# Optimization experiments

Measured on AMD Instinct MI355X. Metric: run time of the kernel, lower is better.

The kernel has to match this reference:

```python
import jax, jax.numpy as jnp
import numpy as np

B, S, D = 2, 2048, 1024
H = 16
HD = D // H  # head_dim = 64


def _xavier(key, shape):
    fan_out, fan_in = shape
    bound = jnp.sqrt(6.0 / (fan_in + fan_out))
    return jax.random.uniform(key, shape, jnp.float32, -bound, bound)


def setup_inputs() -> dict:
    key = jax.random.key(0)
    kx, kqkv, ko = jax.random.split(key, 3)
    x = jax.random.normal(kx, (B, S, D), jnp.float32)
    # torch nn.Linear stores weight as [out, in]; we keep that layout and use x @ W.T
    W_qkv = _xavier(kqkv, (3 * D, D))
    b_qkv = jnp.zeros((3 * D,), jnp.float32)
    W_o = _xavier(ko, (D, D))
    b_o = jnp.zeros((D,), jnp.float32)
    return {"x": x, "W_qkv": W_qkv, "b_qkv": b_qkv, "W_o": W_o, "b_o": b_o}


def reference(x, W_qkv, b_qkv, W_o, b_o):
    b, s, d = x.shape
    h, hd = H, HD
    # qkv projection: [b, s, 3d]
    qkv = jnp.einsum("bsd,ed->bse", x, W_qkv) + b_qkv
    # [b, s, h, 3*hd] -> [b, h, s, 3*hd]
    qkv = qkv.reshape(b, s, h, 3 * hd).transpose(0, 2, 1, 3)
    q, k, v = jnp.split(qkv, 3, axis=-1)
    scale = 1.0 / jnp.sqrt(jnp.asarray(hd, x.dtype))
    logits = jnp.einsum("bhqd,bhkd->bhqk", q, k) * scale
    attn = jax.nn.softmax(logits, axis=-1)
    values = jnp.einsum("bhqk,bhkd->bhqd", attn, v)
    values = values.transpose(0, 2, 1, 3).reshape(b, s, d)
    return jnp.einsum("bsd,ed->bse", values, W_o) + b_o
```

## Files before the change

kernel.cpp:

```cpp
#include <hip/hip_runtime.h>

typedef unsigned short u16;
typedef __attribute__((ext_vector_type(8))) short bf16x8;
typedef __attribute__((ext_vector_type(4))) float f32x4;
typedef __attribute__((ext_vector_type(16))) float f32x16;
typedef __attribute__((ext_vector_type(4))) unsigned short u16x4;

__device__ __forceinline__ u16 f2bf(float f) {
    unsigned u = __float_as_uint(f);
    u = u + 0x7FFFu + ((u >> 16) & 1u);
    return (u16)(u >> 16);
}

__device__ __forceinline__ void gload16(const void* g, void* l) {
    __builtin_amdgcn_global_load_lds(
        (const __attribute__((address_space(1))) unsigned int*)g,
        (__attribute__((address_space(3))) unsigned int*)l,
        16, 0, 0);
}

__device__ __forceinline__ f32x4 mfma16(bf16x8 a, bf16x8 b, f32x4 c) {
    return __builtin_amdgcn_mfma_f32_16x16x32_bf16(a, b, c, 0, 0, 0);
}
__device__ __forceinline__ f32x16 mfma32(bf16x8 a, bf16x8 b, f32x16 c) {
    return __builtin_amdgcn_mfma_f32_32x32x16_bf16(a, b, c, 0, 0, 0);
}

__global__ __launch_bounds__(256) void cvt_all(const float* __restrict__ x,
                                               const float* __restrict__ wqkv,
                                               const float* __restrict__ wo,
                                               u16* __restrict__ dst) {
    int i = blockIdx.x * 256 + threadIdx.x;
    float4 v;
    if (i < 1048576)       v = ((const float4*)x)[i];
    else if (i < 1835008)  v = ((const float4*)wqkv)[i - 1048576];
    else                   v = ((const float4*)wo)[i - 1835008];
    u16x4 o = { f2bf(v.x), f2bf(v.y), f2bf(v.z), f2bf(v.w) };
    ((u16x4*)dst)[i] = o;
}

template <int BM, int BN, bool OUT_BF16>
__global__ __launch_bounds__(256) void gemm_bt(const u16* __restrict__ A,
                                               const u16* __restrict__ Bm,
                                               const float* __restrict__ bias,
                                               void* __restrict__ Cp,
                                               int M, int N, int K) {
    constexpr int FM = BM / 32, FN = BN / 32;
    __shared__ u16 As[2][BM * 64];
    __shared__ u16 Bs[2][BN * 64];
    const int tid = threadIdx.x, lane = tid & 63, wave = tid >> 6;
    const int wr = wave >> 1, wc = wave & 1;
    const int l15 = lane & 15, l4 = lane >> 4;

    const int nx = gridDim.x, nwg = nx * gridDim.y;
    const int id = blockIdx.y * nx + blockIdx.x;
    const int wg = (id & 7) * (nwg >> 3) + (id >> 3);
    const int m0 = (wg / nx) * BM, n0 = (wg % nx) * BN;

    f32x4 zero = {0.f, 0.f, 0.f, 0.f};
    f32x4 acc[FM][FN];
#pragma unroll
    for (int m = 0; m < FM; ++m)
#pragma unroll
        for (int n = 0; n < FN; ++n) acc[m][n] = zero;

#define STAGE_BT(tt, buf) {                                                 \
    _Pragma("unroll")                                                       \
    for (int i = 0; i < BM / 32; ++i) {                                     \
        int c = i * 256 + tid;                                              \
        int r = c >> 3, kc = (c & 7) ^ (r & 7);                             \
        gload16(A + (size_t)(m0 + r) * K + (tt) * 64 + kc * 8,              \
                &As[buf][(i * 256 + wave * 64) * 8]);                       \
    }                                                                       \
    _Pragma("unroll")                                                       \
    for (int i = 0; i < BN / 32; ++i) {                                     \
        int c = i * 256 + tid;                                              \
        int r = c >> 3, kc = (c & 7) ^ (r & 7);                             \
        gload16(Bm + (size_t)(n0 + r) * K + (tt) * 64 + kc * 8,             \
                &Bs[buf][(i * 256 + wave * 64) * 8]);                       \
    } }

    const int nt = K >> 6;
    STAGE_BT(0, 0);
    for (int t = 0; t < nt; ++t) {
        asm volatile("s_waitcnt vmcnt(0)" ::: "memory");
        asm volatile("s_barrier" ::: "memory");
        if (t < nt - 1) { STAGE_BT(t + 1, (t + 1) & 1); }
        const char* Asb = (const char*)As[t & 1];
        const char* Bsb = (const char*)Bs[t & 1];
#pragma unroll
        for (int kk = 0; kk < 2; ++kk) {
            bf16x8 af[FM], bfr[FN];
#pragma unroll
            for (int m = 0; m < FM; ++m) {
                int row = wr * (BM / 2) + m * 16 + l15;
                int ch = (kk * 4 + l4) ^ (row & 7);
                af[m] = *(const bf16x8*)(Asb + row * 128 + ch * 16);
            }
#pragma unroll
            for (int n = 0; n < FN; ++n) {
                int row = wc * (BN / 2) + n * 16 + l15;
                int ch = (kk * 4 + l4) ^ (row & 7);
                bfr[n] = *(const bf16x8*)(Bsb + row * 128 + ch * 16);
            }
#pragma unroll
            for (int m = 0; m < FM; ++m)
#pragma unroll
                for (int n = 0; n < FN; ++n)
                    acc[m][n] = mfma16(af[m], bfr[n], acc[m][n]);
        }
    }
#undef STAGE_BT
    float bv[FN];
#pragma unroll
    for (int n = 0; n < FN; ++n) bv[n] = bias[n0 + wc * (BN / 2) + n * 16 + l15];
#pragma unroll
    for (int m = 0; m < FM; ++m) {
#pragma unroll
        for (int j = 0; j < 4; ++j) {
            size_t row = (size_t)(m0 + wr * (BM / 2) + m * 16 + l4 * 4 + j);
#pragma unroll
            for (int n = 0; n < FN; ++n) {
                int col = n0 + wc * (BN / 2) + n * 16 + l15;
                float v = acc[m][n][j] + bv[n];
                if (OUT_BF16)
                    ((u16*)Cp)[row * (size_t)N + col] = f2bf(v);
                else
                    ((float*)Cp)[row * (size_t)N + col] = v;
            }
        }
    }
}

__global__ __launch_bounds__(512) void gemm192(const u16* __restrict__ A,
                                               const u16* __restrict__ Bm,
                                               const float* __restrict__ bias,
                                               u16* __restrict__ Cp,
                                               u16* __restrict__ Vt,
                                               int M, int N, int K) {
    __shared__ __align__(16) char lds[114688];
    const int tid = threadIdx.x, lane = tid & 63, wave = tid >> 6;
    const int wr = wave >> 2, wc = wave & 3;
    const int l15 = lane & 15, l4 = lane >> 4;

    const int nx = gridDim.x, nwg = nx * gridDim.y;
    const int id = blockIdx.y * nx + blockIdx.x;
    const int wg = (id & 7) * (nwg >> 3) + (id >> 3);
    const int m0 = (wg / nx) * 256, n0 = (wg % nx) * 192;

    const u16* asrc[2][2];
#pragma unroll
    for (int q = 0; q < 2; ++q)
#pragma unroll
        for (int r = 0; r < 2; ++r) {
            int c = r * 512 + tid;
            int lr = c >> 3;
            int kc = (c & 7) ^ (lr & 7);
            asrc[q][r] = A + (size_t)(m0 + lr + (lr & 64) + q * 64) * K + kc * 8;
        }
    const u16* bsrc[3];
    {
        int lr2 = tid >> 3;
        int kc = (tid & 7) ^ (lr2 & 7);
#pragma unroll
        for (int r3 = 0; r3 < 3; ++r3)
            bsrc[r3] = Bm + (size_t)(n0 + r3 * 64 + lr2) * K + kc * 8;
    }
    const int sd0 = wave * 1024;
    const int sd1 = 8192 + wave * 1024;

    const int roA = (wr * 64 + l15) * 128;
    const int roB = (wc * 16 + l15) * 128;
    int ch16[2];
#pragma unroll
    for (int kk = 0; kk < 2; ++kk) ch16[kk] = ((kk * 4 + l4) ^ (l15 & 7)) * 16;

    f32x4 zero = {0.f, 0.f, 0.f, 0.f};
    f32x4 acc[2][3][4];
#pragma unroll
    for (int a = 0; a < 2; ++a)
#pragma unroll
        for (int b = 0; b < 3; ++b)
#pragma unroll
            for (int c = 0; c < 4; ++c) acc[a][b][c] = zero;

#define STG_A(q, tt) { char* rb = lds + (((tt) & 1) * 32768) + (q) * 16384;           \
        gload16(asrc[q][0] + (size_t)(tt) * 64, rb + sd0);                             \
        gload16(asrc[q][1] + (size_t)(tt) * 64, rb + sd1); }
#define STG_B(r3, tt) { char* rb = lds + 65536 + (((tt) & 1) * 24576) + (r3) * 8192;  \
        gload16(bsrc[r3] + (size_t)(tt) * 64, rb + wave * 1024); }
#define MFMA_G(MH, TH, AF) {                                                           \
        _Pragma("unroll")                                                              \
        for (int fm = 0; fm < 4; ++fm)                                                 \
            _Pragma("unroll")                                                          \
            for (int kk = 0; kk < 2; ++kk)                                             \
                acc[MH][TH][fm] = mfma16(AF[fm][kk], bfr[TH][kk], acc[MH][TH][fm]); }

    STG_A(0, 0); STG_B(0, 0); STG_B(1, 0); STG_A(1, 0); STG_B(2, 0);
    asm volatile("s_waitcnt vmcnt(3)" ::: "memory");
    asm volatile("s_barrier" ::: "memory");

    bf16x8 af0[4][2], af1[4][2], bfr[3][2];
    const int nt = K >> 6;
    for (int t = 0; t < nt; ++t) {
        const char* Ab = lds + (t & 1) * 32768;
        const char* Bb = lds + 65536 + (t & 1) * 24576;
#pragma unroll
        for (int fm = 0; fm < 4; ++fm)
#pragma unroll
            for (int kk = 0; kk < 2; ++kk)
                af0[fm][kk] = *(const bf16x8*)(Ab + roA + fm * 2048 + ch16[kk]);
#pragma unroll
        for (int th = 0; th < 2; ++th)
#pragma unroll
            for (int kk = 0; kk < 2; ++kk)
                bfr[th][kk] = *(const bf16x8*)(Bb + th * 8192 + roB + ch16[kk]);
        if (t < nt - 1) { STG_A(0, t + 1); STG_B(0, t + 1); STG_B(1, t + 1); }
        asm volatile("s_barrier" ::: "memory");
        __builtin_amdgcn_s_setprio(1);
        MFMA_G(0, 0, af0); MFMA_G(0, 1, af0);
        __builtin_amdgcn_s_setprio(0);
        if (t < nt - 1) asm volatile("s_waitcnt vmcnt(4)" ::: "memory");
        else            asm volatile("s_waitcnt vmcnt(0)" ::: "memory");
        asm volatile("s_barrier" ::: "memory");
#pragma unroll
        for (int fm = 0; fm < 4; ++fm)
#pragma unroll
            for (int kk = 0; kk < 2; ++kk)
                af1[fm][kk] = *(const bf16x8*)(Ab + 16384 + roA + fm * 2048 + ch16[kk]);
#pragma unroll
        for (int kk = 0; kk < 2; ++kk)
            bfr[2][kk] = *(const bf16x8*)(Bb + 2 * 8192 + roB + ch16[kk]);
        if (t < nt - 1) { STG_A(1, t + 1); }
        asm volatile("s_barrier" ::: "memory");
        __builtin_amdgcn_s_setprio(1);
        MFMA_G(0, 2, af0); MFMA_G(1, 0, af1);
        __builtin_amdgcn_s_setprio(0);
        asm volatile("s_barrier" ::: "memory");
        if (t < nt - 1) { STG_B(2, t + 1); }
        asm volatile("s_barrier" ::: "memory");
        __builtin_amdgcn_s_setprio(1);
        MFMA_G(1, 1, af1); MFMA_G(1, 2, af1);
        __builtin_amdgcn_s_setprio(0);
        if (t < nt - 1) asm volatile("s_waitcnt vmcnt(3)" ::: "memory");
        asm volatile("s_barrier" ::: "memory");
    }
#undef STG_A
#undef STG_B
#undef MFMA_G

    float bv[3];
#pragma unroll
    for (int th = 0; th < 3; ++th) bv[th] = bias[n0 + th * 64 + wc * 16 + l15];
#pragma unroll
    for (int mh = 0; mh < 2; ++mh)
#pragma unroll
        for (int fm = 0; fm < 4; ++fm)
#pragma unroll
            for (int j = 0; j < 4; ++j) {
                size_t row = (size_t)(m0 + wr * 128 + mh * 64 + fm * 16 + l4 * 4 + j);
#pragma unroll
                for (int th = 0; th < 3; ++th) {
                    int col = n0 + th * 64 + wc * 16 + l15;
                    Cp[row * (size_t)N + col] = f2bf(acc[mh][th][fm][j] + bv[th]);
                }
            }

    const int b_ = m0 >> 11, s0_ = m0 & 2047;
    const int h = n0 / 192;
    const int vl = wc * 16 + l15;
#pragma unroll
    for (int mh = 0; mh < 2; ++mh)
#pragma unroll
        for (int fm = 0; fm < 4; ++fm) {
            int r0 = wr * 128 + mh * 64 + fm * 16 + l4 * 4;
            u16x4 w = { f2bf(acc[mh][2][fm][0] + bv[2]),
                        f2bf(acc[mh][2][fm][1] + bv[2]),
                        f2bf(acc[mh][2][fm][2] + bv[2]),
                        f2bf(acc[mh][2][fm][3] + bv[2]) };
            *(u16x4*)(lds + vl * 520 + r0 * 2) = w;
        }
    __syncthreads();
    {
        size_t vt_base = ((size_t)(b_ * 16 + h) * 64) * 2048 + s0_;
        for (int c = tid; c < 4096; c += 512) {
            int vl2 = c >> 6, sl = c & 63;
            u16x4 w = *(const u16x4*)(lds + vl2 * 520 + sl * 8);
            *(u16x4*)(Vt + (size_t)vl2 * 2048 + vt_base + sl * 4) = w;
        }
    }
}

__global__ __launch_bounds__(512, 4) void attn_kernel(const u16* __restrict__ qkv,
                                                      const u16* __restrict__ Vt,
                                                      u16* __restrict__ vals) {
    __shared__ __align__(16) char lds[65536];
    const int L = blockIdx.x;
    const int ord = L >> 3;
    const int hb = (L & 7) * 4 + (ord >> 4);
    const int qt = ord & 15;
    const int h = hb & 15, b = hb >> 4;
    const int st8 = (ord & 1) << 3;
    const int tid = threadIdx.x, lane = tid & 63, wave = tid >> 6;
    const int gtid = tid & 255, qsub = wave & 3, kvh = wave >> 2;
    const int l31 = lane & 31, hi = lane >> 5;
    const float S2E = 0.18033688f;

    const u16* qbase = qkv + (size_t)(b * 2048 + qt * 128 + qsub * 32 + l31) * 3072 + h * 192;
    bf16x8 Qf[4];
#pragma unroll
    for (int ks = 0; ks < 4; ++ks) {
        bf16x8 q = *(const bf16x8*)(qbase + ks * 16 + hi * 8);
#pragma unroll
        for (int j = 0; j < 8; ++j) {
            float f = __uint_as_float(((unsigned)(u16)q[j]) << 16) * S2E;
            q[j] = (short)f2bf(f);
        }
        Qf[ks] = q;
    }

    const u16* kpb[2];
    const u16* vpb[2];
    int dst[2];
#pragma unroll
    for (int i = 0; i < 2; ++i) {
        int c = i * 256 + gtid;
        int fi = c >> 6, dl = c & 63;
        int mm = fi >> 2, ks = fi & 3;
        int row = mm * 32 + (dl & 31);
        int col = ks * 16 + (dl >> 5) * 8;
        kpb[i] = qkv + (size_t)(b * 2048 + kvh * 1024 + row) * 3072 + h * 192 + 64 + col;
        vpb[i] = Vt + ((size_t)((b * 16 + h) * 64 + row)) * 2048 + kvh * 1024 + col;
        dst[i] = fi * 512;
    }
    u16* Kst = (u16*)lds + kvh * 8192;
    u16* Vst = (u16*)lds + 16384 + kvh * 8192;

    f32x16 accO[2];
#pragma unroll
    for (int md = 0; md < 2; ++md)
#pragma unroll
        for (int r = 0; r < 16; ++r) accO[md][r] = 0.f;
    float accLs = 0.f;

    const char* KsL = (const char*)Kst + lane * 16;
    const char* VsL = (const char*)Vst + lane * 16;

#pragma unroll
    for (int i = 0; i < 2; ++i) gload16(kpb[i] + (size_t)st8 * 196608, Kst + dst[i]);
#pragma unroll
    for (int i = 0; i < 2; ++i) gload16(vpb[i] + (size_t)st8 * 64, Vst + dst[i]);

    for (int t = 0; t < 16; ++t) {
        asm volatile("s_waitcnt vmcnt(0)" ::: "memory");
        asm volatile("s_barrier" ::: "memory");

        if (t < 15) {
            int phys = (t + 1 + st8) & 15;
            u16* kd = Kst + ((t + 1) & 1) * 4096;
            u16* vd = Vst + ((t + 1) & 1) * 4096;
#pragma unroll
            for (int i = 0; i < 2; ++i) gload16(kpb[i] + (size_t)phys * 196608, kd + dst[i]);
#pragma unroll
            for (int i = 0; i < 2; ++i) gload16(vpb[i] + (size_t)phys * 64, vd + dst[i]);
        }

        const char* Kb = KsL + (t & 1) * 8192;
        const char* Vb = VsL + (t & 1) * 8192;

        f32x16 sc[2];
        __builtin_amdgcn_s_setprio(1);
#pragma unroll
        for (int m = 0; m < 2; ++m) {
            f32x16 c;
#pragma unroll
            for (int r = 0; r < 16; ++r) c[r] = 0.f;
#pragma unroll
            for (int ks = 0; ks < 4; ++ks) {
                bf16x8 kf = *(const bf16x8*)(Kb + (m * 4 + ks) * 1024);
                c = mfma32(kf, Qf[ks], c);
            }
            sc[m] = c;
        }
        __builtin_amdgcn_s_setprio(0);

        bf16x8 Pf[4];
#pragma unroll
        for (int r = 0; r < 16; ++r)
            sc[0][r] = __builtin_amdgcn_exp2f(sc[0][r]);
        {
            float q0 = (sc[0][0] + sc[0][1]) + (sc[0][2] + sc[0][3]);
            float q1 = (sc[0][4] + sc[0][5]) + (sc[0][6] + sc[0][7]);
            float q2 = (sc[0][8] + sc[0][9]) + (sc[0][10] + sc[0][11]);
            float q3 = (sc[0][12] + sc[0][13]) + (sc[0][14] + sc[0][15]);
            accLs += (q0 + q1) + (q2 + q3);
        }
        {
            unsigned W0[4], W1[4];
#pragma unroll
            for (int g = 0; g < 4; ++g) {
                asm("v_cvt_pk_bf16_f32 %0, %1, %2"
                    : "=v"(W0[g]) : "v"(sc[0][4 * g + 0]), "v"(sc[0][4 * g + 1]));
                asm("v_cvt_pk_bf16_f32 %0, %1, %2"
                    : "=v"(W1[g]) : "v"(sc[0][4 * g + 2]), "v"(sc[0][4 * g + 3]));
            }
#pragma unroll
            for (int kpair = 0; kpair < 2; ++kpair) {
                unsigned xa = W0[2 * kpair], ya = W0[2 * kpair + 1];
                unsigned xb = W1[2 * kpair], yb = W1[2 * kpair + 1];
                asm volatile("v_permlane32_swap_b32 %0, %1" : "+v"(xa), "+v"(ya));
                asm volatile("v_permlane32_swap_b32 %0, %1" : "+v"(xb), "+v"(yb));
                union { unsigned w[4]; bf16x8 v; } u;
                u.w[0] = xa; u.w[1] = xb; u.w[2] = ya; u.w[3] = yb;
                Pf[kpair] = u.v;
            }
        }

        __builtin_amdgcn_s_setprio(1);
#pragma unroll
        for (int md = 0; md < 2; ++md) {
            f32x16 c = accO[md];
#pragma unroll
            for (int ks = 0; ks < 2; ++ks) {
                bf16x8 vf = *(const bf16x8*)(Vb + (md * 4 + ks) * 1024);
                c = mfma32(vf, Pf[ks], c);
            }
            accO[md] = c;
        }
        __builtin_amdgcn_s_setprio(0);

#pragma unroll
        for (int r = 0; r < 16; ++r)
            sc[1][r] = __builtin_amdgcn_exp2f(sc[1][r]);
        {
            float q0 = (sc[1][0] + sc[1][1]) + (sc[1][2] + sc[1][3]);
            float q1 = (sc[1][4] + sc[1][5]) + (sc[1][6] + sc[1][7]);
            float q2 = (sc[1][8] + sc[1][9]) + (sc[1][10] + sc[1][11]);
            float q3 = (sc[1][12] + sc[1][13]) + (sc[1][14] + sc[1][15]);
            accLs += (q0 + q1) + (q2 + q3);
        }
        {
            unsigned W0[4], W1[4];
#pragma unroll
            for (int g = 0; g < 4; ++g) {
                asm("v_cvt_pk_bf16_f32 %0, %1, %2"
                    : "=v"(W0[g]) : "v"(sc[1][4 * g + 0]), "v"(sc[1][4 * g + 1]));
                asm("v_cvt_pk_bf16_f32 %0, %1, %2"
                    : "=v"(W1[g]) : "v"(sc[1][4 * g + 2]), "v"(sc[1][4 * g + 3]));
            }
#pragma unroll
            for (int kpair = 0; kpair < 2; ++kpair) {
                unsigned xa = W0[2 * kpair], ya = W0[2 * kpair + 1];
                unsigned xb = W1[2 * kpair], yb = W1[2 * kpair + 1];
                asm volatile("v_permlane32_swap_b32 %0, %1" : "+v"(xa), "+v"(ya));
                asm volatile("v_permlane32_swap_b32 %0, %1" : "+v"(xb), "+v"(yb));
                union { unsigned w[4]; bf16x8 v; } u;
                u.w[0] = xa; u.w[1] = xb; u.w[2] = ya; u.w[3] = yb;
                Pf[2 + kpair] = u.v;
            }
        }

        __builtin_amdgcn_s_setprio(1);
#pragma unroll
        for (int md = 0; md < 2; ++md) {
            f32x16 c = accO[md];
#pragma unroll
            for (int ks = 2; ks < 4; ++ks) {
                bf16x8 vf = *(const bf16x8*)(Vb + (md * 4 + ks) * 1024);
                c = mfma32(vf, Pf[ks], c);
            }
            accO[md] = c;
        }
        __builtin_amdgcn_s_setprio(0);
    }

    float lt;
    {
        float xa = accLs, xb = accLs;
        asm volatile("v_permlane32_swap_b32 %0, %1" : "+v"(xa), "+v"(xb));
        lt = xa + xb;
    }

    float* MO = (float*)lds;
    float* ML = (float*)(lds + 32768);
    __syncthreads();
    if (kvh == 1) {
        int r = qsub * 64 + lane;
#pragma unroll
        for (int md = 0; md < 2; ++md)
#pragma unroll
            for (int g = 0; g < 4; ++g)
#pragma unroll
                for (int j = 0; j < 4; ++j)
                    MO[(md * 16 + 4 * g + j) * 256 + r] = accO[md][4 * g + j];
        ML[r] = lt;
    }
    __syncthreads();
    if (kvh == 0) {
        int r = qsub * 64 + lane;
        float inv = 1.f / (lt + ML[r]);
        size_t rowoff = (size_t)(b * 2048 + qt * 128 + qsub * 32 + l31) * 1024 + h * 64;
#pragma unroll
        for (int md = 0; md < 2; ++md)
#pragma unroll
            for (int g = 0; g < 4; ++g) {
                float w0 = MO[(md * 16 + 4 * g + 0) * 256 + r];
                float w1 = MO[(md * 16 + 4 * g + 1) * 256 + r];
                float w2 = MO[(md * 16 + 4 * g + 2) * 256 + r];
                float w3 = MO[(md * 16 + 4 * g + 3) * 256 + r];
                u16x4 o = { f2bf((accO[md][4 * g + 0] + w0) * inv),
                            f2bf((accO[md][4 * g + 1] + w1) * inv),
                            f2bf((accO[md][4 * g + 2] + w2) * inv),
                            f2bf((accO[md][4 * g + 3] + w3) * inv) };
                *(u16x4*)(vals + rowoff + md * 32 + 8 * g + 4 * hi) = o;
            }
    }
}

extern "C" void kernel_launch(void* const* d_in, const int* in_sizes, int n_in,
                              void* d_out, int out_size, void* d_ws, size_t ws_size,
                              hipStream_t stream) {
    const float* x    = (const float*)d_in[0];
    const float* Wqkv = (const float*)d_in[1];
    const float* bqkv = (const float*)d_in[2];
    const float* Wo   = (const float*)d_in[3];
    const float* bo   = (const float*)d_in[4];
    float* out = (float*)d_out;

    char* ws = (char*)d_ws;
    u16* x_bf    = (u16*)(ws);
    u16* Wqkv_bf = (u16*)(ws + 8388608);
    u16* Wo_bf   = (u16*)(ws + 14680064);
    u16* qkv_bf  = (u16*)(ws + 16777216);
    u16* Vt      = (u16*)(ws + 41943040);
    u16* vals    = (u16*)(ws + 50331648);

    cvt_all<<<8192, 256, 0, stream>>>(x, Wqkv, Wo, x_bf);

    gemm192<<<dim3(16, 16), 512, 0, stream>>>(x_bf, Wqkv_bf, bqkv, qkv_bf, Vt,
                                              4096, 3072, 1024);

    attn_kernel<<<512, 512, 0, stream>>>(qkv_bf, Vt, vals);

    gemm_bt<128, 64, false><<<dim3(16, 32), 256, 0, stream>>>(vals, Wo_bf, bo,
                                                              (void*)out, 4096, 1024, 1024);
}
```

Before: 105.8 us.

## Replace output projection GEMM with 256x64 tile, split-phase pipelined kernel

Swaps the generic 128x64 double-buffered output-projection GEMM for a 512-thread 256x64 tile kernel modeled on the QKV GEMM. It splits the A tile into two halves loaded and consumed in alternating phases with partial vmcnt waits, and raises wave priority around the MFMA blocks so loads overlap compute. The aim is better B-tile reuse and latency hiding. The cost is that the grid shrinks from 512 to 256 workgroups, which may leave compute units idle on a small GEMM.

New measurement: 105.0 us (median of 3 runs). No clear change (-0.7%).

```diff
diff --git a/kernel.cpp b/kernel.cpp
--- a/kernel.cpp
+++ b/kernel.cpp
@@ -39,99 +39,6 @@
     ((u16x4*)dst)[i] = o;
 }
 
-template <int BM, int BN, bool OUT_BF16>
-__global__ __launch_bounds__(256) void gemm_bt(const u16* __restrict__ A,
-                                               const u16* __restrict__ Bm,
-                                               const float* __restrict__ bias,
-                                               void* __restrict__ Cp,
-                                               int M, int N, int K) {
-    constexpr int FM = BM / 32, FN = BN / 32;
-    __shared__ u16 As[2][BM * 64];
-    __shared__ u16 Bs[2][BN * 64];
-    const int tid = threadIdx.x, lane = tid & 63, wave = tid >> 6;
-    const int wr = wave >> 1, wc = wave & 1;
-    const int l15 = lane & 15, l4 = lane >> 4;
-
-    const int nx = gridDim.x, nwg = nx * gridDim.y;
-    const int id = blockIdx.y * nx + blockIdx.x;
-    const int wg = (id & 7) * (nwg >> 3) + (id >> 3);
-    const int m0 = (wg / nx) * BM, n0 = (wg % nx) * BN;
-
-    f32x4 zero = {0.f, 0.f, 0.f, 0.f};
-    f32x4 acc[FM][FN];
-#pragma unroll
-    for (int m = 0; m < FM; ++m)
-#pragma unroll
-        for (int n = 0; n < FN; ++n) acc[m][n] = zero;
-
-#define STAGE_BT(tt, buf) {                                                 \
-    _Pragma("unroll")                                                       \
-    for (int i = 0; i < BM / 32; ++i) {                                     \
-        int c = i * 256 + tid;                                              \
-        int r = c >> 3, kc = (c & 7) ^ (r & 7);                             \
-        gload16(A + (size_t)(m0 + r) * K + (tt) * 64 + kc * 8,              \
-                &As[buf][(i * 256 + wave * 64) * 8]);                       \
-    }                                                                       \
-    _Pragma("unroll")                                                       \
-    for (int i = 0; i < BN / 32; ++i) {                                     \
-        int c = i * 256 + tid;                                              \
-        int r = c >> 3, kc = (c & 7) ^ (r & 7);                             \
-        gload16(Bm + (size_t)(n0 + r) * K + (tt) * 64 + kc * 8,             \
-                &Bs[buf][(i * 256 + wave * 64) * 8]);                       \
-    } }
-
-    const int nt = K >> 6;
-    STAGE_BT(0, 0);
-    for (int t = 0; t < nt; ++t) {
-        asm volatile("s_waitcnt vmcnt(0)" ::: "memory");
-        asm volatile("s_barrier" ::: "memory");
-        if (t < nt - 1) { STAGE_BT(t + 1, (t + 1) & 1); }
-        const char* Asb = (const char*)As[t & 1];
-        const char* Bsb = (const char*)Bs[t & 1];
-#pragma unroll
-        for (int kk = 0; kk < 2; ++kk) {
-            bf16x8 af[FM], bfr[FN];
-#pragma unroll
-            for (int m = 0; m < FM; ++m) {
-                int row = wr * (BM / 2) + m * 16 + l15;
-                int ch = (kk * 4 + l4) ^ (row & 7);
-                af[m] = *(const bf16x8*)(Asb + row * 128 + ch * 16);
-            }
-#pragma unroll
-            for (int n = 0; n < FN; ++n) {
-                int row = wc * (BN / 2) + n * 16 + l15;
-                int ch = (kk * 4 + l4) ^ (row & 7);
-                bfr[n] = *(const bf16x8*)(Bsb + row * 128 + ch * 16);
-            }
-#pragma unroll
-            for (int m = 0; m < FM; ++m)
-#pragma unroll
-                for (int n = 0; n < FN; ++n)
-                    acc[m][n] = mfma16(af[m], bfr[n], acc[m][n]);
-        }
-    }
-#undef STAGE_BT
-    float bv[FN];
-#pragma unroll
-    for (int n = 0; n < FN; ++n) bv[n] = bias[n0 + wc * (BN / 2) + n * 16 + l15];
-#pragma unroll
-    for (int m = 0; m < FM; ++m) {
-#pragma unroll
-        for (int j = 0; j < 4; ++j) {
-            size_t row = (size_t)(m0 + wr * (BM / 2) + m * 16 + l4 * 4 + j);
-#pragma unroll
-            for (int n = 0; n < FN; ++n) {
-                int col = n0 + wc * (BN / 2) + n * 16 + l15;
-                float v = acc[m][n][j] + bv[n];
-                if (OUT_BF16)
-                    ((u16*)Cp)[row * (size_t)N + col] = f2bf(v);
-                else
-                    ((float*)Cp)[row * (size_t)N + col] = v;
-            }
-        }
-    }
-}
-
 __global__ __launch_bounds__(512) void gemm192(const u16* __restrict__ A,
                                                const u16* __restrict__ Bm,
                                                const float* __restrict__ bias,
@@ -289,6 +196,121 @@
             *(u16x4*)(Vt + (size_t)vl2 * 2048 + vt_base + sl * 4) = w;
         }
     }
+}
+
+__global__ __launch_bounds__(512) void gemm_out(const u16* __restrict__ A,
+                                                const u16* __restrict__ Bm,
+                                                const float* __restrict__ bias,
+                                                float* __restrict__ Cp,
+                                                int M, int N, int K) {
+    __shared__ __align__(16) char lds[81920];
+    const int tid = threadIdx.x, lane = tid & 63, wave = tid >> 6;
+    const int wr = wave >> 2, wc = wave & 3;
+    const int l15 = lane & 15, l4 = lane >> 4;
+
+    const int nx = gridDim.x, nwg = nx * gridDim.y;
+    const int id = blockIdx.y * nx + blockIdx.x;
+    const int wg = (id & 7) * (nwg >> 3) + (id >> 3);
+    const int m0 = (wg / nx) * 256, n0 = (wg % nx) * 64;
+
+    const u16* asrc[2][2];
+#pragma unroll
+    for (int q = 0; q < 2; ++q)
+#pragma unroll
+        for (int r = 0; r < 2; ++r) {
+            int c = r * 512 + tid;
+            int lr = c >> 3;
+            int kc = (c & 7) ^ (lr & 7);
+            asrc[q][r] = A + (size_t)(m0 + lr + (lr & 64) + q * 64) * K + kc * 8;
+        }
+    const u16* bsrc;
+    {
+        int lr2 = tid >> 3;
+        int kc = (tid & 7) ^ (lr2 & 7);
+        bsrc = Bm + (size_t)(n0 + lr2) * K + kc * 8;
+    }
+    const int sd0 = wave * 1024;
+    const int sd1 = 8192 + wave * 1024;
+
+    const int roA = (wr * 64 + l15) * 128;
+    const int roB = (wc * 16 + l15) * 128;
+    int ch16[2];
+#pragma unroll
+    for (int kk = 0; kk < 2; ++kk) ch16[kk] = ((kk * 4 + l4) ^ (l15 & 7)) * 16;
+
+    f32x4 zero = {0.f, 0.f, 0.f, 0.f};
+    f32x4 acc[2][4];
+#pragma unroll
+    for (int a = 0; a < 2; ++a)
+#pragma unroll
+        for (int c = 0; c < 4; ++c) acc[a][c] = zero;
+
+#define SGA(q, tt) { char* rb = lds + (((tt) & 1) * 32768) + (q) * 16384;   \
+        gload16(asrc[q][0] + (size_t)(tt) * 64, rb + sd0);                   \
+        gload16(asrc[q][1] + (size_t)(tt) * 64, rb + sd1); }
+#define SGB(tt) { char* rb = lds + 65536 + (((tt) & 1) * 8192);              \
+        gload16(bsrc + (size_t)(tt) * 64, rb + wave * 1024); }
+
+    SGA(0, 0); SGB(0); SGA(1, 0);
+    asm volatile("s_waitcnt vmcnt(2)" ::: "memory");
+    asm volatile("s_barrier" ::: "memory");
+
+    bf16x8 af0[4][2], af1[4][2], bfr[2];
+    const int nt = K >> 6;
+    for (int t = 0; t < nt; ++t) {
+        const char* Ab = lds + (t & 1) * 32768;
+        const char* Bb = lds + 65536 + (t & 1) * 8192;
+#pragma unroll
+        for (int fm = 0; fm < 4; ++fm)
+#pragma unroll
+            for (int kk = 0; kk < 2; ++kk)
+                af0[fm][kk] = *(const bf16x8*)(Ab + roA + fm * 2048 + ch16[kk]);
+#pragma unroll
+        for (int kk = 0; kk < 2; ++kk)
+            bfr[kk] = *(const bf16x8*)(Bb + roB + ch16[kk]);
+        if (t < nt - 1) { SGA(0, t + 1); SGB(t + 1); }
+        asm volatile("s_barrier" ::: "memory");
+        __builtin_amdgcn_s_setprio(1);
+#pragma unroll
+        for (int fm = 0; fm < 4; ++fm)
+#pragma unroll
+            for (int kk = 0; kk < 2; ++kk)
+                acc[0][fm] = mfma16(af0[fm][kk], bfr[kk], acc[0][fm]);
+        __builtin_amdgcn_s_setprio(0);
+        if (t < nt - 1) asm volatile("s_waitcnt vmcnt(3)" ::: "memory");
+        else            asm volatile("s_waitcnt vmcnt(0)" ::: "memory");
+        asm volatile("s_barrier" ::: "memory");
+#pragma unroll
+        for (int fm = 0; fm < 4; ++fm)
+#pragma unroll
+            for (int kk = 0; kk < 2; ++kk)
+                af1[fm][kk] = *(const bf16x8*)(Ab + 16384 + roA + fm * 2048 + ch16[kk]);
+        if (t < nt - 1) { SGA(1, t + 1); }
+        asm volatile("s_barrier" ::: "memory");
+        __builtin_amdgcn_s_setprio(1);
+#pragma unroll
+        for (int fm = 0; fm < 4; ++fm)
+#pragma unroll
+            for (int kk = 0; kk < 2; ++kk)
+                acc[1][fm] = mfma16(af1[fm][kk], bfr[kk], acc[1][fm]);
+        __builtin_amdgcn_s_setprio(0);
+        if (t < nt - 1) asm volatile("s_waitcnt vmcnt(2)" ::: "memory");
+        asm volatile("s_barrier" ::: "memory");
+    }
+#undef SGA
+#undef SGB
+
+    float bv = bias[n0 + wc * 16 + l15];
+#pragma unroll
+    for (int mh = 0; mh < 2; ++mh)
+#pragma unroll
+        for (int fm = 0; fm < 4; ++fm)
+#pragma unroll
+            for (int j = 0; j < 4; ++j) {
+                size_t row = (size_t)(m0 + wr * 128 + mh * 64 + fm * 16 + l4 * 4 + j);
+                int col = n0 + wc * 16 + l15;
+                Cp[row * (size_t)N + col] = acc[mh][fm][j] + bv;
+            }
 }
 
 __global__ __launch_bounds__(512, 4) void attn_kernel(const u16* __restrict__ qkv,
@@ -542,6 +564,6 @@
 
     attn_kernel<<<512, 512, 0, stream>>>(qkv_bf, Vt, vals);
 
-    gemm_bt<128, 64, false><<<dim3(16, 32), 256, 0, stream>>>(vals, Wo_bf, bo,
-                                                              (void*)out, 4096, 1024, 1024);
-}
+    gemm_out<<<dim3(16, 16), 512, 0, stream>>>(vals, Wo_bf, bo, out,
+                                               4096, 1024, 1024);
+}
```
